# Kernel tuning notes

Hardware: AMD Instinct MI355X
Metric: run time of the kernel (lower is better)

The kernel has to match this reference:

```python
import jax, jax.numpy as jnp
import numpy as np

NUM_NODES = 100000
HIDDEN = 128
HEADS = 4
NUM_EDGES = 1600000
NUM_PAIRS = 100000


def _leaky_relu(x, slope=0.2):
    return jnp.where(x >= 0, x, slope * x)


def _gat_layer(x, W, a_src, a_dst, src, dst):
    # x: [N, D]; W: [D, H*Dh]; a_src/a_dst: [H, Dh]
    N = x.shape[0]
    H, Dh = a_src.shape
    h = (x @ W).reshape(N, H, Dh)
    hs = h[src]                                   # [E, H, Dh] gather
    e = _leaky_relu((hs * a_src).sum(-1) + (h[dst] * a_dst).sum(-1))  # [E, H]
    # torch scatter_reduce amax over a zeros buffer => max clamped at 0
    m = jnp.maximum(jax.ops.segment_max(e, dst, num_segments=N), 0.0)  # [N, H]
    a = jnp.exp(e - m[dst])
    s = jax.ops.segment_sum(a, dst, num_segments=N)
    a = a / (s[dst] + 1e-10)
    out = jax.ops.segment_sum(hs * a[..., None], dst, num_segments=N)  # [N, H, Dh]
    return out.reshape(N, H * Dh)


def setup_inputs() -> dict:
    key = jax.random.key(0)
    ks = jax.random.split(key, 16)
    N, D, H = NUM_NODES, HIDDEN, HEADS
    Dh = D // H
    sW = float(np.sqrt(6.0 / (D + D)))
    sa = float(np.sqrt(6.0 / (H + Dh)))
    inp = {
        'embed': jax.random.uniform(ks[0], (N, D), jnp.float32, -sW, sW),
        'W1': jax.random.uniform(ks[1], (D, D), jnp.float32, -sW, sW),
        'a_src1': jax.random.uniform(ks[2], (H, Dh), jnp.float32, -sa, sa),
        'a_dst1': jax.random.uniform(ks[3], (H, Dh), jnp.float32, -sa, sa),
        'W2': jax.random.uniform(ks[4], (D, D), jnp.float32, -sW, sW),
        'a_src2': jax.random.uniform(ks[5], (H, Dh), jnp.float32, -sa, sa),
        'a_dst2': jax.random.uniform(ks[6], (H, Dh), jnp.float32, -sa, sa),
        'lp_w1': jax.random.uniform(ks[7], (2 * D, D), jnp.float32, -sW, sW),
        'lp_b1': jnp.zeros((D,), jnp.float32),
        'lp_w2': jax.random.uniform(ks[8], (D, 1), jnp.float32, -sW, sW),
        'lp_b2': jnp.zeros((1,), jnp.float32),
        'edge_index': jax.random.randint(ks[9], (2, NUM_EDGES), 0, N, jnp.int64 if jax.config.jax_enable_x64 else jnp.int32),
        'link_src': jax.random.randint(ks[10], (NUM_PAIRS,), 0, N),
        'link_dst': jax.random.randint(ks[11], (NUM_PAIRS,), 0, N),
    }
    return inp


def reference(embed, W1, a_src1, a_dst1, W2, a_src2, a_dst2,
              lp_w1, lp_b1, lp_w2, lp_b2, edge_index, link_src, link_dst):
    src, dst = edge_index[0], edge_index[1]
    x = embed
    x = jax.nn.elu(_gat_layer(x, W1, a_src1, a_dst1, src, dst)) + x
    x = jax.nn.elu(_gat_layer(x, W2, a_src2, a_dst2, src, dst)) + x
    z = x
    hcat = jnp.concatenate([z[link_src], z[link_dst]], axis=-1)  # [P, 2D]
    hid = jax.nn.relu(hcat @ lp_w1 + lp_b1)
    logits = (hid @ lp_w2 + lp_b2).squeeze(-1)  # [P]
    return logits
```

## Files before the change

### kernel.cpp

```cpp
#include <hip/hip_runtime.h>

typedef unsigned short u16;
typedef unsigned int u32;
typedef __attribute__((ext_vector_type(8))) short short8;
typedef __attribute__((ext_vector_type(4))) float float4v;

#define N_NODES 100000
#define N_EDGES 1600000
#define N_PAIRS 100000
#define NBUCKP 256
#define NB_USED 196
#define BUCK_CAP 8704
#define BIN_GRID 391

__device__ __forceinline__ float bf2f(u32 lo16) {
    union { u32 u; float f; } v;
    v.u = lo16 << 16;
    return v.f;
}
__device__ __forceinline__ u16 f2bf(float f) {
    union { float f; u32 u; } v;
    v.f = f;
    u32 r = v.u + 0x7fffu + ((v.u >> 16) & 1u);
    return (u16)(r >> 16);
}

#define FMIX_LO(A, Q, W) asm("v_fma_mix_f32 %0, %1, %2, %0 op_sel:[0,0,0] op_sel_hi:[1,1,0]" : "+v"(A) : "v"(Q), "v"(W))
#define FMIX_HI(A, Q, W) asm("v_fma_mix_f32 %0, %1, %2, %0 op_sel:[1,0,0] op_sel_hi:[1,1,0]" : "+v"(A) : "v"(Q), "v"(W))

__global__ __launch_bounds__(256) void k_prepB4(const float* __restrict__ W1, const float* __restrict__ W2,
                                                const float* __restrict__ WA, const float* __restrict__ WB,
                                                u16* __restrict__ B1, u16* __restrict__ B2,
                                                u16* __restrict__ BA, u16* __restrict__ BB,
                                                int* __restrict__ bucket_cur) {
    if (blockIdx.x == 32) {
        bucket_cur[threadIdx.x] = threadIdx.x * BUCK_CAP;
        return;
    }
    int w = blockIdx.x >> 3;
    const float* W = (w == 0) ? W1 : (w == 1) ? W2 : (w == 2) ? WA : WB;
    u16* Bf = (w == 0) ? B1 : (w == 1) ? B2 : (w == 2) ? BA : BB;
    int t = (blockIdx.x & 7) * 256 + threadIdx.x;
    int kk = t >> 9, tn = (t >> 6) & 7, quad = (t >> 4) & 3, l15 = t & 15;
#pragma unroll
    for (int j = 0; j < 8; j++) {
        int k = kk * 32 + quad * 8 + j;
        int n = tn * 16 + l15;
        Bf[(size_t)t * 8 + j] = f2bf(W[k * 128 + n]);
    }
}

__global__ __launch_bounds__(256) void k_bin(const int* __restrict__ esrc, const int* __restrict__ edst,
                                             int* bucket_cur, int2* __restrict__ binned) {
    __shared__ int cnt[NBUCKP];
    __shared__ int base[NBUCKP];
    int t = threadIdx.x;
    cnt[t] = 0;
    __syncthreads();
    int s[16], d[16], r[16];
    int e0 = blockIdx.x * 4096;
#pragma unroll
    for (int k = 0; k < 16; k++) {
        int e = e0 + k * 256 + t;
        if (e < N_EDGES) {
            s[k] = esrc[e];
            d[k] = edst[e];
            r[k] = atomicAdd(&cnt[d[k] >> 9], 1);
        } else {
            d[k] = -1;
        }
    }
    __syncthreads();
    base[t] = cnt[t] ? atomicAdd(&bucket_cur[t], cnt[t]) : 0;
    __syncthreads();
#pragma unroll
    for (int k = 0; k < 16; k++) {
        if (d[k] >= 0) {
            int bk = d[k] >> 9;
            int pos = base[bk] + r[k];
            if (pos < (bk + 1) * BUCK_CAP)
                binned[pos] = make_int2(s[k], d[k]);
        }
    }
}

__global__ __launch_bounds__(512) void k_sort(const int2* __restrict__ binned,
                                              const int* __restrict__ bucket_cur,
                                              int* __restrict__ row_ptr,
                                              int* __restrict__ col_src) {
    __shared__ int cnt[512];
    __shared__ int sm[512];
    int b = blockIdx.x, t = threadIdx.x;

    int partial = 0;
    if (t < b) partial = bucket_cur[t] - t * BUCK_CAP;
    sm[t] = partial;
    __syncthreads();
    for (int o = 256; o >= 1; o >>= 1) {
        if (t < o) sm[t] += sm[t + o];
        __syncthreads();
    }
    int base = sm[0];
    int n_e = bucket_cur[b] - b * BUCK_CAP;
    if (n_e > BUCK_CAP) n_e = BUCK_CAP;
    __syncthreads();

    cnt[t] = 0;
    __syncthreads();
    const int2* ebase = binned + (size_t)b * BUCK_CAP;
    for (int i = t; i < n_e; i += 512)
        atomicAdd(&cnt[ebase[i].y & 511], 1);
    __syncthreads();
    int v = cnt[t];
    sm[t] = v;
    __syncthreads();
    for (int o = 1; o < 512; o <<= 1) {
        int x = (t >= o) ? sm[t - o] : 0;
        __syncthreads();
        sm[t] += x;
        __syncthreads();
    }
    int excl = base + sm[t] - v;
    int node = b * 512 + t;
    if (node <= N_NODES) row_ptr[node] = excl;
    cnt[t] = excl;
    __syncthreads();
    for (int i = t; i < n_e; i += 512) {
        int2 sd = ebase[i];
        int p = atomicAdd(&cnt[sd.y & 511], 1);
        col_src[p] = sd.x;
    }
}

template<bool AF32, bool QUANT>
__global__ __launch_bounds__(256) void k_gemm(const void* __restrict__ Ap,
                                              const u16* __restrict__ Bf,
                                              u16* __restrict__ C,
                                              char* __restrict__ hq,
                                              float* __restrict__ alsc,
                                              const float* __restrict__ a_src,
                                              const float* __restrict__ a_dst,
                                              float* __restrict__ al_d, int M) {
    int wave = threadIdx.x >> 6, lane = threadIdx.x & 63;
    int quad = lane >> 4, l15 = lane & 15;
    int row0 = blockIdx.x * 64 + wave * 16;
    int m = row0 + l15;
    int mload = (m < M) ? m : (M - 1);

    short8 a[4];
    if (AF32) {
        const float* A = (const float*)Ap;
#pragma unroll
        for (int kk = 0; kk < 4; kk++) {
            const float* p = A + (size_t)mload * 128 + kk * 32 + quad * 8;
            float4 f0 = *(const float4*)p;
            float4 f1 = *(const float4*)(p + 4);
            short8 av;
            av[0] = (short)f2bf(f0.x); av[1] = (short)f2bf(f0.y);
            av[2] = (short)f2bf(f0.z); av[3] = (short)f2bf(f0.w);
            av[4] = (short)f2bf(f1.x); av[5] = (short)f2bf(f1.y);
            av[6] = (short)f2bf(f1.z); av[7] = (short)f2bf(f1.w);
            a[kk] = av;
        }
    } else {
        const u16* A = (const u16*)Ap;
#pragma unroll
        for (int kk = 0; kk < 4; kk++)
            a[kk] = *(const short8*)(A + (size_t)mload * 128 + kk * 32 + quad * 8);
    }

    float4v acc[8];
#pragma unroll
    for (int tn = 0; tn < 8; tn++) acc[tn] = (float4v){0.f, 0.f, 0.f, 0.f};

#pragma unroll
    for (int kk = 0; kk < 4; kk++) {
#pragma unroll
        for (int tn = 0; tn < 8; tn++) {
            short8 b = *(const short8*)(Bf + ((size_t)((kk * 8 + tn) * 64 + lane)) * 8);
            acc[tn] = __builtin_amdgcn_mfma_f32_16x16x32_bf16(a[kk], b, acc[tn], 0, 0, 0);
        }
    }

    float as0[4], as1[4], ad0[4], ad1[4];
    if (QUANT) {
#pragma unroll
        for (int hd = 0; hd < 4; hd++) {
            as0[hd] = a_src[hd * 32 + l15];
            as1[hd] = a_src[hd * 32 + 16 + l15];
            ad0[hd] = a_dst[hd * 32 + l15];
            ad1[hd] = a_dst[hd * 32 + 16 + l15];
        }
    }

#pragma unroll
    for (int rg = 0; rg < 4; rg++) {
        int gr = row0 + quad * 4 + rg;
        bool ok = (gr < M);
        if (!QUANT) {
            if (ok) {
#pragma unroll
                for (int tn = 0; tn < 8; tn++)
                    C[(size_t)gr * 128 + tn * 16 + l15] = f2bf(acc[tn][rg]);
            }
        } else {
            float amax = 0.f;
#pragma unroll
            for (int tn = 0; tn < 8; tn++) amax = fmaxf(amax, fabsf(acc[tn][rg]));
#pragma unroll
            for (int mm = 1; mm < 16; mm <<= 1) amax = fmaxf(amax, __shfl_xor(amax, mm, 64));
            float inv_s = (amax > 0.f) ? 127.f / amax : 0.f;
            if (ok) {
#pragma unroll
                for (int tn = 0; tn < 8; tn++) {
                    int q = (int)rintf(acc[tn][rg] * inv_s);
                    hq[(size_t)gr * 128 + tn * 16 + l15] = (char)(q + 128);
                }
            }
            float ps[4], pd[4];
#pragma unroll
            for (int hd = 0; hd < 4; hd++) {
                float c0 = acc[2 * hd][rg];
                float c1 = acc[2 * hd + 1][rg];
                ps[hd] = c0 * as0[hd] + c1 * as1[hd];
                pd[hd] = c0 * ad0[hd] + c1 * ad1[hd];
            }
#pragma unroll
            for (int mm = 1; mm < 16; mm <<= 1) {
#pragma unroll
                for (int hd = 0; hd < 4; hd++) {
                    ps[hd] += __shfl_xor(ps[hd], mm, 64);
                    pd[hd] += __shfl_xor(pd[hd], mm, 64);
                }
            }
            if (ok && l15 < 4) {
                float vs = (l15 == 0) ? ps[0] : (l15 == 1) ? ps[1] : (l15 == 2) ? ps[2] : ps[3];
                float vd = (l15 == 0) ? pd[0] : (l15 == 1) ? pd[1] : (l15 == 2) ? pd[2] : pd[3];
                alsc[(size_t)gr * 8 + l15 * 2]     = vs;
                alsc[(size_t)gr * 8 + l15 * 2 + 1] = amax * (1.f / 127.f);
                al_d[gr * 4 + l15] = vd;
            }
        }
    }
}

template<bool XF32>
__global__ __launch_bounds__(256) void k_agg(const int* __restrict__ row_ptr, const int* __restrict__ col_src,
                      const float* __restrict__ alsc, const float* __restrict__ al_d,
                      const char* __restrict__ hq,
                      const void* __restrict__ xin, u16* __restrict__ xout) {
    int node = blockIdx.x * 4 + (threadIdx.x >> 6);
    int lane = threadIdx.x & 63;
    int l15 = lane & 15;
    int grp = lane >> 4;
    int bh  = l15 >> 2;
    int ae  = lane >> 2;
    int ah  = lane & 3;
    int beg = row_ptr[node], end = row_ptr[node + 1];
    int deg = end - beg;
    int degm1 = (deg > 0) ? deg - 1 : 0;
    float adst = al_d[node * 4 + ah];
    u32 loff = (u32)(l15 * 8);

    float sw = 0.f, swl = 0.f;
    u32 h_one = 0x3C00u;
    float acc[8];
#pragma unroll
    for (int k = 0; k < 8; k++) acc[k] = 0.f;

    int nch = (deg + 15) >> 4;
    for (int cb = 0; cb < nch; cb++) {
        int c = cb * 16;
        int idx = c + l15;
        idx = (idx <= degm1) ? idx : degm1;
        int sv = col_src[beg + idx];

        int sA = __shfl(sv, ae, 64);
        float2 av = *(const float2*)(alsc + ((size_t)sA << 3) + (ah << 1));
        float ev = av.x + adst;
        ev = fmaxf(ev, 0.2f * ev);
        float w = __expf(ev);
        w = ((c + ae) < deg) ? w : 0.f;
        sw += w;
        float wsc = w * av.y;

#pragma unroll
        for (int i = 0; i < 4; i++) {
            int slot = 4 * i + grp;
            int s = __shfl(sv, slot, 64);
            float wl = __shfl(wsc, slot * 4 + bh, 64);
            u32 wlh;
            asm("v_cvt_f16_f32 %0, %1" : "=v"(wlh) : "v"(wl));
            FMIX_LO(swl, h_one, wlh);
            u32 off = ((u32)s << 7) + loff;
            uint2 hv = *(const uint2*)(hq + off);
            u32 p01 = __builtin_amdgcn_perm(0x64646464u, hv.x, 0x04010400u);
            u32 p23 = __builtin_amdgcn_perm(0x64646464u, hv.x, 0x04030402u);
            u32 p45 = __builtin_amdgcn_perm(0x64646464u, hv.y, 0x04010400u);
            u32 p67 = __builtin_amdgcn_perm(0x64646464u, hv.y, 0x04030402u);
            FMIX_LO(acc[0], p01, wlh); FMIX_HI(acc[1], p01, wlh);
            FMIX_LO(acc[2], p23, wlh); FMIX_HI(acc[3], p23, wlh);
            FMIX_LO(acc[4], p45, wlh); FMIX_HI(acc[5], p45, wlh);
            FMIX_LO(acc[6], p67, wlh); FMIX_HI(acc[7], p67, wlh);
        }
    }

#pragma unroll
    for (int k = 0; k < 8; k++) acc[k] = fmaf(swl, -1152.f, acc[k]);

#pragma unroll
    for (int mm = 4; mm < 64; mm <<= 1) sw += __shfl_xor(sw, mm, 64);
    float inv = 1.f / (__shfl(sw, bh, 64) + 1e-10f);

#pragma unroll
    for (int k = 0; k < 8; k++) {
        acc[k] += __shfl_xor(acc[k], 16, 64);
        acc[k] += __shfl_xor(acc[k], 32, 64);
    }

    if (grp == 0) {
        float r[8];
        if (XF32) {
            const float* x = (const float*)xin;
            float4 x0 = *(const float4*)&x[(size_t)node * 128 + l15 * 8];
            float4 x1 = *(const float4*)&x[(size_t)node * 128 + l15 * 8 + 4];
            r[0] = x0.x; r[1] = x0.y; r[2] = x0.z; r[3] = x0.w;
            r[4] = x1.x; r[5] = x1.y; r[6] = x1.z; r[7] = x1.w;
        } else {
            const u16* x = (const u16*)xin;
            short8 xv = *(const short8*)&x[(size_t)node * 128 + l15 * 8];
#pragma unroll
            for (int k = 0; k < 8; k++) r[k] = bf2f((u16)xv[k]);
        }
        u32 ow[4];
#pragma unroll
        for (int k = 0; k < 4; k++) {
            float a0 = acc[2 * k] * inv;
            float a1 = acc[2 * k + 1] * inv;
            a0 = (a0 > 0.f) ? a0 : (__expf(a0) - 1.f);
            a1 = (a1 > 0.f) ? a1 : (__expf(a1) - 1.f);
            ow[k] = (u32)f2bf(a0 + r[2 * k]) | ((u32)f2bf(a1 + r[2 * k + 1]) << 16);
        }
        *(uint4*)&xout[(size_t)node * 128 + l15 * 8] = make_uint4(ow[0], ow[1], ow[2], ow[3]);
    }
}

__global__ __launch_bounds__(256) void k_link(const int* __restrict__ psrc, const int* __restrict__ pdst,
                                              const u16* __restrict__ z,
                                              const u16* __restrict__ BfA, const u16* __restrict__ BfB,
                                              const float* __restrict__ b1, const float* __restrict__ w2,
                                              const float* __restrict__ b2, float* __restrict__ out) {
    int wave = threadIdx.x >> 6, lane = threadIdx.x & 63;
    int quad = lane >> 4, l15 = lane & 15;
    int row0 = blockIdx.x * 64 + wave * 16;
    int prow = row0 + l15;
    int pload = (prow < N_PAIRS) ? prow : (N_PAIRS - 1);
    int s = psrc[pload], d = pdst[pload];

    short8 a1[4], a2[4];
#pragma unroll
    for (int kk = 0; kk < 4; kk++) {
        a1[kk] = *(const short8*)(z + (size_t)s * 128 + kk * 32 + quad * 8);
        a2[kk] = *(const short8*)(z + (size_t)d * 128 + kk * 32 + quad * 8);
    }

    float4v acc[8];
#pragma unroll
    for (int tn = 0; tn < 8; tn++) acc[tn] = (float4v){0.f, 0.f, 0.f, 0.f};

#pragma unroll
    for (int kk = 0; kk < 4; kk++) {
#pragma unroll
        for (int tn = 0; tn < 8; tn++) {
            short8 ba = *(const short8*)(BfA + ((size_t)((kk * 8 + tn) * 64 + lane)) * 8);
            acc[tn] = __builtin_amdgcn_mfma_f32_16x16x32_bf16(a1[kk], ba, acc[tn], 0, 0, 0);
            short8 bb = *(const short8*)(BfB + ((size_t)((kk * 8 + tn) * 64 + lane)) * 8);
            acc[tn] = __builtin_amdgcn_mfma_f32_16x16x32_bf16(a2[kk], bb, acc[tn], 0, 0, 0);
        }
    }

    float b1v[8], w2v[8];
#pragma unroll
    for (int tn = 0; tn < 8; tn++) {
        b1v[tn] = b1[tn * 16 + l15];
        w2v[tn] = w2[tn * 16 + l15];
    }
    float bb2 = b2[0];

#pragma unroll
    for (int rg = 0; rg < 4; rg++) {
        float part = 0.f;
#pragma unroll
        for (int tn = 0; tn < 8; tn++) {
            float h = acc[tn][rg] + b1v[tn];
            h = (h > 0.f) ? h : 0.f;
            part += h * w2v[tn];
        }
#pragma unroll
        for (int mm = 1; mm < 16; mm <<= 1) part += __shfl_xor(part, mm, 64);
        int gr = row0 + quad * 4 + rg;
        if (l15 == 0 && gr < N_PAIRS) out[gr] = part + bb2;
    }
}

extern "C" void kernel_launch(void* const* d_in, const int* in_sizes, int n_in,
                              void* d_out, int out_size, void* d_ws, size_t ws_size,
                              hipStream_t stream) {
    const float* embed  = (const float*)d_in[0];
    const float* W1     = (const float*)d_in[1];
    const float* a_src1 = (const float*)d_in[2];
    const float* a_dst1 = (const float*)d_in[3];
    const float* W2     = (const float*)d_in[4];
    const float* a_src2 = (const float*)d_in[5];
    const float* a_dst2 = (const float*)d_in[6];
    const float* lp_w1  = (const float*)d_in[7];
    const float* lp_b1  = (const float*)d_in[8];
    const float* lp_w2  = (const float*)d_in[9];
    const float* lp_b2  = (const float*)d_in[10];
    const int*   edge   = (const int*)d_in[11];
    const int*   lsrc   = (const int*)d_in[12];
    const int*   ldst   = (const int*)d_in[13];
    float* out = (float*)d_out;

    char* ws = (char*)d_ws;
    size_t off = 0;
    auto alloc = [&](size_t bytes) -> char* {
        char* p = ws + off;
        off += (bytes + 255) & ~(size_t)255;
        return p;
    };
    int*  row_ptr    = (int*)alloc((N_NODES + 1) * 4);
    int*  bucket_cur = (int*)alloc(NBUCKP * 4);
    int2* binned     = (int2*)alloc((size_t)NBUCKP * BUCK_CAP * 8);
    int*  col_src    = (int*)alloc((size_t)N_EDGES * 4);
    char* hq         = (char*)alloc((size_t)N_NODES * 128);
    float* alsc      = (float*)alloc((size_t)N_NODES * 8 * 4);
    float* al_d      = (float*)alloc((size_t)N_NODES * 4 * 4);
    u16*  x1         = (u16*)alloc((size_t)N_NODES * 128 * 2);
    u16*  z          = (u16*)alloc((size_t)N_NODES * 128 * 2);
    u16*  Bf1        = (u16*)alloc(128 * 128 * 2);
    u16*  Bf2        = (u16*)alloc(128 * 128 * 2);
    u16*  BfA        = (u16*)alloc(128 * 128 * 2);
    u16*  BfB        = (u16*)alloc(128 * 128 * 2);

    const int* esrc = edge;
    const int* edst = edge + N_EDGES;
    const int GB = (N_NODES + 63) / 64;
    const int GP = (N_PAIRS + 63) / 64;

    k_prepB4<<<33, 256, 0, stream>>>(W1, W2, lp_w1, lp_w1 + 128 * 128, Bf1, Bf2, BfA, BfB, bucket_cur);

    k_bin <<<BIN_GRID, 256, 0, stream>>>(esrc, edst, bucket_cur, binned);
    k_sort<<<NB_USED, 512, 0, stream>>>(binned, bucket_cur, row_ptr, col_src);

    k_gemm<true, true><<<GB, 256, 0, stream>>>(embed, Bf1, nullptr,
                                               hq, alsc, a_src1, a_dst1, al_d, N_NODES);
    k_agg<true><<<N_NODES / 4, 256, 0, stream>>>(row_ptr, col_src, alsc, al_d, hq, embed, x1);
    k_gemm<false, true><<<GB, 256, 0, stream>>>(x1, Bf2, nullptr,
                                                hq, alsc, a_src2, a_dst2, al_d, N_NODES);
    k_agg<false><<<N_NODES / 4, 256, 0, stream>>>(row_ptr, col_src, alsc, al_d, hq, x1, z);
    k_link<<<GP, 256, 0, stream>>>(lsrc, ldst, z, BfA, BfB, lp_b1, lp_w2, lp_b2, out);
}
```

Before: 328.7 us.

## Pack binned edges into 32-bit words and use smaller 256-node buckets

```diff
diff --git a/kernel.cpp b/kernel.cpp
--- a/kernel.cpp
+++ b/kernel.cpp
@@ -8,9 +8,8 @@
 #define N_NODES 100000
 #define N_EDGES 1600000
 #define N_PAIRS 100000
-#define NBUCKP 256
-#define NB_USED 196
-#define BUCK_CAP 8704
+#define NBUCK 391
+#define BUCK_CAP 4608
 #define BIN_GRID 391
 
 __device__ __forceinline__ float bf2f(u32 lo16) {
@@ -34,7 +33,8 @@
                                                 u16* __restrict__ BA, u16* __restrict__ BB,
                                                 int* __restrict__ bucket_cur) {
     if (blockIdx.x == 32) {
-        bucket_cur[threadIdx.x] = threadIdx.x * BUCK_CAP;
+        for (int i = threadIdx.x; i < NBUCK; i += 256)
+            bucket_cur[i] = i * BUCK_CAP;
         return;
     }
     int w = blockIdx.x >> 3;
@@ -51,11 +51,11 @@
 }
 
 __global__ __launch_bounds__(256) void k_bin(const int* __restrict__ esrc, const int* __restrict__ edst,
-                                             int* bucket_cur, int2* __restrict__ binned) {
-    __shared__ int cnt[NBUCKP];
-    __shared__ int base[NBUCKP];
+                                             int* bucket_cur, u32* __restrict__ binned) {
+    __shared__ int cnt[NBUCK];
+    __shared__ int base[NBUCK];
     int t = threadIdx.x;
-    cnt[t] = 0;
+    for (int i = t; i < NBUCK; i += 256) cnt[i] = 0;
     __syncthreads();
     int s[16], d[16], r[16];
     int e0 = blockIdx.x * 4096;
@@ -65,38 +65,42 @@
         if (e < N_EDGES) {
             s[k] = esrc[e];
             d[k] = edst[e];
-            r[k] = atomicAdd(&cnt[d[k] >> 9], 1);
+            r[k] = atomicAdd(&cnt[d[k] >> 8], 1);
         } else {
             d[k] = -1;
         }
     }
     __syncthreads();
-    base[t] = cnt[t] ? atomicAdd(&bucket_cur[t], cnt[t]) : 0;
+    for (int i = t; i < NBUCK; i += 256)
+        base[i] = cnt[i] ? atomicAdd(&bucket_cur[i], cnt[i]) : 0;
     __syncthreads();
 #pragma unroll
     for (int k = 0; k < 16; k++) {
         if (d[k] >= 0) {
-            int bk = d[k] >> 9;
+            int bk = d[k] >> 8;
             int pos = base[bk] + r[k];
             if (pos < (bk + 1) * BUCK_CAP)
-                binned[pos] = make_int2(s[k], d[k]);
-        }
-    }
-}
-
-__global__ __launch_bounds__(512) void k_sort(const int2* __restrict__ binned,
+                binned[pos] = ((u32)s[k] << 8) | ((u32)d[k] & 255u);
+        }
+    }
+}
+
+__global__ __launch_bounds__(256) void k_sort(const u32* __restrict__ binned,
                                               const int* __restrict__ bucket_cur,
                                               int* __restrict__ row_ptr,
                                               int* __restrict__ col_src) {
-    __shared__ int cnt[512];
-    __shared__ int sm[512];
+    __shared__ int cnt[256];
+    __shared__ int sm[256];
     int b = blockIdx.x, t = threadIdx.x;
 
     int partial = 0;
-    if (t < b) partial = bucket_cur[t] - t * BUCK_CAP;
+    for (int i = t; i < b; i += 256) {
+        int c = bucket_cur[i] - i * BUCK_CAP;
+        partial += (c > BUCK_CAP) ? BUCK_CAP : c;
+    }
     sm[t] = partial;
     __syncthreads();
-    for (int o = 256; o >= 1; o >>= 1) {
+    for (int o = 128; o >= 1; o >>= 1) {
         if (t < o) sm[t] += sm[t + o];
         __syncthreads();
     }
@@ -107,28 +111,35 @@
 
     cnt[t] = 0;
     __syncthreads();
-    const int2* ebase = binned + (size_t)b * BUCK_CAP;
-    for (int i = t; i < n_e; i += 512)
-        atomicAdd(&cnt[ebase[i].y & 511], 1);
+    const u32* ebase = binned + (size_t)b * BUCK_CAP;
+    u32 ed[18];
+#pragma unroll
+    for (int j = 0; j < 18; j++) {
+        int i = t + j * 256;
+        ed[j] = (i < n_e) ? ebase[i] : 0xFFFFFFFFu;
+        if (ed[j] != 0xFFFFFFFFu) atomicAdd(&cnt[ed[j] & 255u], 1);
+    }
     __syncthreads();
     int v = cnt[t];
     sm[t] = v;
     __syncthreads();
-    for (int o = 1; o < 512; o <<= 1) {
+    for (int o = 1; o < 256; o <<= 1) {
         int x = (t >= o) ? sm[t - o] : 0;
         __syncthreads();
         sm[t] += x;
         __syncthreads();
     }
     int excl = base + sm[t] - v;
-    int node = b * 512 + t;
+    int node = b * 256 + t;
     if (node <= N_NODES) row_ptr[node] = excl;
     cnt[t] = excl;
     __syncthreads();
-    for (int i = t; i < n_e; i += 512) {
-        int2 sd = ebase[i];
-        int p = atomicAdd(&cnt[sd.y & 511], 1);
-        col_src[p] = sd.x;
+#pragma unroll
+    for (int j = 0; j < 18; j++) {
+        if (ed[j] != 0xFFFFFFFFu) {
+            int p = atomicAdd(&cnt[ed[j] & 255u], 1);
+            col_src[p] = (int)(ed[j] >> 8);
+        }
     }
 }
 
@@ -430,8 +441,8 @@
         return p;
     };
     int*  row_ptr    = (int*)alloc((N_NODES + 1) * 4);
-    int*  bucket_cur = (int*)alloc(NBUCKP * 4);
-    int2* binned     = (int2*)alloc((size_t)NBUCKP * BUCK_CAP * 8);
+    int*  bucket_cur = (int*)alloc(512 * 4);
+    u32*  binned     = (u32*)alloc((size_t)NBUCK * BUCK_CAP * 4);
     int*  col_src    = (int*)alloc((size_t)N_EDGES * 4);
     char* hq         = (char*)alloc((size_t)N_NODES * 128);
     float* alsc      = (float*)alloc((size_t)N_NODES * 8 * 4);
@@ -451,7 +462,7 @@
     k_prepB4<<<33, 256, 0, stream>>>(W1, W2, lp_w1, lp_w1 + 128 * 128, Bf1, Bf2, BfA, BfB, bucket_cur);
 
     k_bin <<<BIN_GRID, 256, 0, stream>>>(esrc, edst, bucket_cur, binned);
-    k_sort<<<NB_USED, 512, 0, stream>>>(binned, bucket_cur, row_ptr, col_src);
+    k_sort<<<NBUCK, 256, 0, stream>>>(binned, bucket_cur, row_ptr, col_src);
 
     k_gemm<true, true><<<GB, 256, 0, stream>>>(embed, Bf1, nullptr,
                                                hq, alsc, a_src1, a_dst1, al_d, N_NODES);
```

After: 326.0 us. About the same (-0.8%).
